# Kernel tuning notes

Measured on AMD Instinct MI355X. Metric: run time of the kernel, lower is better.

The kernel has to match this reference:

```python
import jax, jax.numpy as jnp
import numpy as np

N0, C1, C2 = 100000, 10000, 1000
E0 = 1_600_000
IN = 128
H = 128
OUT = 128


def _pool_edges(ei, ew, cluster, C):
    # PyG pool_edge: remap via cluster, drop self loops, coalesce (sum weights)
    m = cluster[ei]
    mask = m[0] != m[1]
    m = m[:, mask]
    w = ew[mask]
    keys = m[0] * C + m[1]
    uk, inv = np.unique(keys, return_inverse=True)
    w2 = np.bincount(inv, weights=w).astype(np.float32)
    return np.stack([uk // C, uk % C]).astype(np.int64), w2


def _with_self_loops(ei, ew, N):
    # gcn_norm(add_remaining_self_loops, fill_value=1); base edges have no loops
    row = np.concatenate([ei[0], np.arange(N)]).astype(np.int64)
    col = np.concatenate([ei[1], np.arange(N)]).astype(np.int64)
    w = np.concatenate([ew, np.ones(N, np.float32)])
    return row, col, w


def setup_inputs() -> dict:
    rng = np.random.default_rng(0)
    ei = rng.integers(0, N0, size=(2, E0))
    ei = ei[:, ei[0] != ei[1]]
    ew = np.ones(ei.shape[1], np.float32)
    # guaranteed-surjective cluster assignments (stand-in for Louvain output)
    c1 = rng.permutation(np.arange(N0) % C1).astype(np.int64)
    c2 = rng.permutation(np.arange(C1) % C2).astype(np.int64)
    ei1, ew1 = _pool_edges(ei, ew, c1, C1)
    ei2, ew2 = _pool_edges(ei1, ew1, c2, C2)
    r0, co0, w0 = _with_self_loops(ei, ew, N0)
    r1, co1, w1 = _with_self_loops(ei1, ew1, C1)
    r2, co2, w2 = _with_self_loops(ei2, ew2, C2)

    key = jax.random.key(0)
    ks = jax.random.split(key, 16)
    def lin(k, fi, fo):
        return jax.random.normal(k, (fi, fo), jnp.float32) / np.sqrt(fi)
    inp = {
        'x': jax.random.normal(ks[0], (N0, IN), jnp.float32),
        'W_pre': lin(ks[1], IN, H), 'b_pre': jnp.zeros((H,), jnp.float32),
        'W_u0': lin(ks[2], H, H), 'b_u0': jnp.zeros((H,), jnp.float32),
        'W_u1': lin(ks[3], H, H), 'b_u1': jnp.zeros((H,), jnp.float32),
        'W_u2': lin(ks[4], H, H), 'b_u2': jnp.zeros((H,), jnp.float32),
        'W_d0': lin(ks[5], H, OUT), 'b_d0': jnp.zeros((OUT,), jnp.float32),
        'W_d1': lin(ks[6], H, H), 'b_d1': jnp.zeros((H,), jnp.float32),
        'row0': jnp.asarray(r0), 'col0': jnp.asarray(co0), 'ew0': jnp.asarray(w0),
        'row1': jnp.asarray(r1), 'col1': jnp.asarray(co1), 'ew1': jnp.asarray(w1),
        'row2': jnp.asarray(r2), 'col2': jnp.asarray(co2), 'ew2': jnp.asarray(w2),
        'cluster1': jnp.asarray(c1), 'cluster2': jnp.asarray(c2),
    }
    return inp


def _gcn(x, W, b, row, col, ew, N):
    # PyG GCNConv: sym-normalized aggregation at target (col)
    deg = jax.ops.segment_sum(ew, col, num_segments=N)
    dinv = jnp.where(deg > 0, jax.lax.rsqrt(deg), 0.0)
    norm = dinv[row] * ew * dinv[col]
    h = x @ W                                   # [N, F_out]
    out = jax.ops.segment_sum(h[row] * norm[:, None], col, num_segments=N)
    return out + b


def _seg_mean(x, cluster, C):
    s = jax.ops.segment_sum(x, cluster, num_segments=C)
    cnt = jax.ops.segment_sum(jnp.ones((x.shape[0], 1), x.dtype), cluster,
                              num_segments=C)
    return s / jnp.maximum(cnt, 1.0)


def reference(x, W_pre, b_pre, W_u0, b_u0, W_u1, b_u1, W_u2, b_u2,
              W_d0, b_d0, W_d1, b_d1,
              row0, col0, ew0, row1, col1, ew1, row2, col2, ew2,
              cluster1, cluster2):
    # --- up (coarsening) path ---
    h = x @ W_pre + b_pre                                   # preembed
    x0 = jax.nn.relu(_gcn(h, W_u0, b_u0, row0, col0, ew0, N0))
    x1 = _seg_mean(x0, cluster1, C1)                        # avg_pool level 1
    x1 = jax.nn.relu(_gcn(x1, W_u1, b_u1, row1, col1, ew1, C1))
    x2 = _seg_mean(x1, cluster2, C2)                        # avg_pool level 2
    x2 = jax.nn.relu(_gcn(x2, W_u2, b_u2, row2, col2, ew2, C2))
    # --- down (unpooling) path; down convs use all-ones edge weights ---
    y = x1 + x2[cluster2]
    y = jax.nn.relu(_gcn(y, W_d1, b_d1, row1, col1, jnp.ones_like(ew1), C1))
    y = x0 + y[cluster1]
    y = _gcn(y, W_d0, b_d0, row0, col0, jnp.ones_like(ew0), N0)
    return y
```

## Files before the change

### kernel.cpp

```cpp
#include <hip/hip_runtime.h>

#define HH 128
static constexpr int kN0 = 100000;
static constexpr int kC1 = 10000;
static constexpr int kC2 = 1000;

static constexpr int B0 = kN0;
static constexpr int B1 = B0 + kC1;
static constexpr int B2 = B1 + kC2;
static constexpr int B3 = B2 + kC1;
static constexpr int NTOT = B3 + kC2;

static constexpr int NB0 = (kN0 + 127) / 128;
static constexpr int NB1 = (kC1 + 7) / 8;
static constexpr int NB2 = kC2;
static constexpr int NBP1 = (kC1 + 127) / 128;
static constexpr int NBP2 = (kC2 + 15) / 16;
static constexpr int Q0 = NB0;
static constexpr int Q1 = Q0 + NB1;
static constexpr int Q2 = Q1 + NB2;
static constexpr int Q3 = Q2 + NBP1;
static constexpr int NBK = Q3 + NBP2;

__device__ __forceinline__ int bucket_of(int bin) {
  if (bin < B0) return bin >> 7;
  if (bin < B1) return Q0 + ((bin - B0) >> 3);
  if (bin < B2) return Q1 + (bin - B1);
  if (bin < B3) return Q2 + ((bin - B2) >> 7);
  return Q3 + ((bin - B3) >> 4);
}

__device__ __forceinline__ unsigned int f2_to_bf2(float a, float b) {
  unsigned int ua = __float_as_uint(a);
  unsigned int ub = __float_as_uint(b);
  ua = (ua + 0x7fffu + ((ua >> 16) & 1u)) >> 16;
  ub = (ub + 0x7fffu + ((ub >> 16) & 1u)) & 0xffff0000u;
  return ua | ub;
}
__device__ __forceinline__ unsigned short f2bf(float f) {
  unsigned int u = __float_as_uint(f);
  u = (u + 0x7fffu + ((u >> 16) & 1u)) >> 16;
  return (unsigned short)u;
}
__device__ __forceinline__ float bf2f(unsigned short s) {
  return __uint_as_float(((unsigned int)s) << 16);
}

using bf16x8 = __attribute__((ext_vector_type(8))) short;
using f32x4 = __attribute__((ext_vector_type(4))) float;

__global__ __launch_bounds__(256) void p1_kernel(const int* __restrict__ col0,
                                                 const int* __restrict__ col1,
                                                 const int* __restrict__ col2,
                                                 const int* __restrict__ cl1,
                                                 const int* __restrict__ cl2,
                                                 int E0, int E1, int E2,
                                                 int* __restrict__ bucketCnt) {
  __shared__ int h[NBK];
  for (int i = threadIdx.x; i < NBK; i += 256) h[i] = 0;
  __syncthreads();
  int T0 = E0, T1 = T0 + E1, T2 = T1 + E2, T3 = T2 + kN0, T4 = T3 + kC1;
  for (int g = blockIdx.x * 256 + threadIdx.x; g < T4; g += gridDim.x * 256) {
    int bin;
    if (g < T0)      bin = col0[g];
    else if (g < T1) bin = B0 + col1[g - T0];
    else if (g < T2) bin = B1 + col2[g - T1];
    else if (g < T3) bin = B2 + cl1[g - T2];
    else             bin = B3 + cl2[g - T3];
    atomicAdd(&h[bucket_of(bin)], 1);
  }
  __syncthreads();
  for (int i = threadIdx.x; i < NBK; i += 256) {
    int c = h[i];
    if (c) atomicAdd(&bucketCnt[i], c);
  }
}

__global__ __launch_bounds__(1024) void p2_kernel(const int* __restrict__ bucketCnt,
                                                  int* __restrict__ bucketStart,
                                                  int* __restrict__ cursor,
                                                  int* __restrict__ startsg, int T) {
  int t = threadIdx.x;
  int v[4]; int s = 0;
#pragma unroll
  for (int j = 0; j < 4; j++) {
    int i = t * 4 + j;
    v[j] = (i < NBK) ? bucketCnt[i] : 0;
    s += v[j];
  }
  int lane = t & 63, w = t >> 6;
  int incl = s;
  for (int o = 1; o < 64; o <<= 1) { int u = __shfl_up(incl, o); if (lane >= o) incl += u; }
  __shared__ int wt[16];
  if (lane == 63) wt[w] = incl;
  __syncthreads();
  if (t == 0) { int run = 0; for (int i = 0; i < 16; i++) { int c = wt[i]; wt[i] = run; run += c; } }
  __syncthreads();
  int ex = wt[w] + incl - s;
#pragma unroll
  for (int j = 0; j < 4; j++) {
    int i = t * 4 + j;
    if (i < NBK) { bucketStart[i] = ex; cursor[i] = ex; }
    ex += v[j];
  }
  if (t == 0) { bucketStart[NBK] = T; startsg[NTOT] = T; }
}

__global__ __launch_bounds__(256) void p3_kernel(const int* __restrict__ col0,
                                                 const int* __restrict__ col1,
                                                 const int* __restrict__ col2,
                                                 const int* __restrict__ cl1,
                                                 const int* __restrict__ cl2,
                                                 const int* __restrict__ row0,
                                                 const int* __restrict__ row1,
                                                 const int* __restrict__ row2,
                                                 const float* __restrict__ ew1,
                                                 const float* __restrict__ ew2,
                                                 int E0, int E1, int E2,
                                                 int* __restrict__ cursor,
                                                 int4* __restrict__ part) {
  __shared__ int h[NBK];
  __shared__ int gbase[NBK];
  for (int i = threadIdx.x; i < NBK; i += 256) h[i] = 0;
  __syncthreads();
  int T0 = E0, T1 = T0 + E1, T2 = T1 + E2, T3 = T2 + kN0, T4 = T3 + kC1;
  int base = blockIdx.x * 4096;
  int bins[16], srcs[16], rk[16];
  float wv[16];
#pragma unroll
  for (int j = 0; j < 16; j++) {
    int g = base + threadIdx.x + j * 256;
    int bin = -1, src = 0; float w = 0.f;
    if (g < T4) {
      if (g < T0) { bin = col0[g]; src = row0[g]; }
      else if (g < T1) { int e = g - T0; bin = B0 + col1[e]; src = row1[e]; w = ew1[e]; }
      else if (g < T2) { int e = g - T1; bin = B1 + col2[e]; src = row2[e]; w = ew2[e]; }
      else if (g < T3) { int e = g - T2; bin = B2 + cl1[e]; src = e; }
      else             { int e = g - T3; bin = B3 + cl2[e]; src = e; }
    }
    bins[j] = bin; srcs[j] = src; wv[j] = w;
    rk[j] = (bin >= 0) ? atomicAdd(&h[bucket_of(bin)], 1) : 0;
  }
  __syncthreads();
  for (int i = threadIdx.x; i < NBK; i += 256) {
    int c = h[i];
    gbase[i] = c ? atomicAdd(&cursor[i], c) : 0;
  }
  __syncthreads();
#pragma unroll
  for (int j = 0; j < 16; j++) {
    if (bins[j] >= 0) {
      int slot = gbase[bucket_of(bins[j])] + rk[j];
      part[slot] = make_int4(bins[j], srcs[j], __float_as_int(wv[j]), 0);
    }
  }
}

__global__ __launch_bounds__(256) void p4_kernel(const int* __restrict__ bucketStart,
                                                 const int4* __restrict__ part,
                                                 int* __restrict__ startsg,
                                                 int* __restrict__ rowS,
                                                 float* __restrict__ ewSm) {
  int b = blockIdx.x;
  int binLo, width;
  if (b < Q0)      { binLo = b << 7;                 width = 128; if (binLo + width > B0) width = B0 - binLo; }
  else if (b < Q1) { binLo = B0 + ((b - Q0) << 3);   width = 8; }
  else if (b < Q2) { binLo = B1 + (b - Q1);          width = 1; }
  else if (b < Q3) { binLo = B2 + ((b - Q2) << 7);   width = 128; if (binLo + width > B3) width = B3 - binLo; }
  else             { binLo = B3 + ((b - Q3) << 4);   width = 16; if (binLo + width > NTOT) width = NTOT - binLo; }
  int base = bucketStart[b], nend = bucketStart[b + 1];
  int t = threadIdx.x;

  if (width == 1) {
    if (t == 0) startsg[binLo] = base;
    bool isEw = (binLo >= B0 && binLo < B2);
    for (int i = base + t; i < nend; i += 256) {
      int4 it = part[i];
      rowS[i] = it.y;
      if (isEw) ewSm[i] = __int_as_float(it.z);
    }
    return;
  }

  __shared__ int h[128];
  __shared__ int cur[128];
  if (t < 128) h[t] = 0;
  __syncthreads();
  for (int i = base + t; i < nend; i += 256) atomicAdd(&h[part[i].x - binLo], 1);
  __syncthreads();
  if (t == 0) {
    int run = 0;
    for (int j = 0; j < width; j++) {
      cur[j] = run;
      startsg[binLo + j] = base + run;
      run += h[j];
    }
  }
  __syncthreads();
  for (int i = base + t; i < nend; i += 256) {
    int4 it = part[i];
    int k = it.x;
    int r = atomicAdd(&cur[k - binLo], 1);
    int dst = base + r;
    rowS[dst] = it.y;
    if (k >= B0 && k < B2) ewSm[dst] = __int_as_float(it.z);
  }
}

__global__ void dinv_kernel(const int* __restrict__ startsg, const float* __restrict__ ewSm,
                            float* __restrict__ d0, float* __restrict__ d1w,
                            float* __restrict__ d1o, float* __restrict__ d2) {
  int t = blockIdx.x * 256 + threadIdx.x;
  if (t < kN0) {
    int c = startsg[t + 1] - startsg[t];
    d0[t] = c > 0 ? rsqrtf((float)c) : 0.f;
  }
  int wid = t >> 6, lane = t & 63;
  if (wid < kC1) {
    int s = startsg[B0 + wid], e = startsg[B0 + wid + 1];
    float a = 0.f;
    for (int k = s + lane; k < e; k += 64) a += ewSm[k];
    for (int o = 32; o > 0; o >>= 1) a += __shfl_down(a, o);
    if (lane == 0) {
      d1w[wid] = a > 0.f ? rsqrtf(a) : 0.f;
      int c = e - s;
      d1o[wid] = c > 0 ? rsqrtf((float)c) : 0.f;
    }
  } else if (wid < kC1 + kC2) {
    int w2 = wid - kC1;
    int s = startsg[B1 + w2], e = startsg[B1 + w2 + 1];
    float a = 0.f;
    for (int k = s + lane; k < e; k += 64) a += ewSm[k];
    for (int o = 32; o > 0; o >>= 1) a += __shfl_down(a, o);
    if (lane == 0) d2[w2] = a > 0.f ? rsqrtf(a) : 0.f;
  }
}

__global__ void wprep_kernel(const int* __restrict__ rowS, const float* __restrict__ ewSm,
                             const float* __restrict__ d1w, const float* __restrict__ d2,
                             int E0, int E1, int E2,
                             float* __restrict__ wAll) {
  int e = blockIdx.x * 256 + threadIdx.x + E0;
  int tot = E0 + E1 + E2;
  if (e >= tot) return;
  int r = rowS[e];
  if (e < E0 + E1) {
    wAll[e] = d1w[r] * ewSm[e];
  } else {
    wAll[e] = d2[r] * ewSm[e];
  }
}

__global__ __launch_bounds__(256) void matmul_kernel(const float* __restrict__ X,
                                                     const float* __restrict__ Xadd,
                                                     const int* __restrict__ cl,
                                                     const float* __restrict__ W,
                                                     const float* __restrict__ bias,
                                                     const float* __restrict__ rowScale,
                                                     float* __restrict__ Y,
                                                     unsigned int* __restrict__ Ybf, int N) {
  __shared__ float Ws[64 * 128];
  __shared__ float Xs[32 * 128];
  int t = threadIdx.x;
  int rbase = blockIdx.x * 32;
  const float4* X4 = (const float4*)X;
  float4* Xs4 = (float4*)Xs;
#pragma unroll
  for (int i = 0; i < 4; i++) {
    int idx = t + 256 * i;
    int fr = idx >> 5, fc = idx & 31;
    int row = rbase + fr; if (row >= N) row = N - 1;
    float4 v = X4[(size_t)row * 32 + fc];
    if (Xadd) {
      int c = cl[row];
      float4 u = ((const float4*)Xadd)[(size_t)c * 32 + fc];
      v.x += u.x; v.y += u.y; v.z += u.z; v.w += u.w;
    }
    Xs4[idx] = v;
  }
  float acc[4][4];
#pragma unroll
  for (int r = 0; r < 4; r++)
#pragma unroll
    for (int cc = 0; cc < 4; cc++) acc[r][cc] = 0.f;
  int c0 = (t & 31) * 4;
  int rl = (t >> 5) * 4;
  const float4* W4 = (const float4*)W;
  float4* Ws4 = (float4*)Ws;
  for (int half = 0; half < 2; half++) {
    __syncthreads();
#pragma unroll
    for (int i = 0; i < 8; i++) {
      int idx = t + 256 * i;
      Ws4[idx] = W4[half * 2048 + idx];
    }
    __syncthreads();
#pragma unroll 4
    for (int k = 0; k < 64; k++) {
      float4 w4 = *(const float4*)(Ws + k * 128 + c0);
      float xv[4];
#pragma unroll
      for (int r = 0; r < 4; r++) xv[r] = Xs[(rl + r) * 128 + half * 64 + k];
#pragma unroll
      for (int r = 0; r < 4; r++) {
        acc[r][0] = fmaf(xv[r], w4.x, acc[r][0]);
        acc[r][1] = fmaf(xv[r], w4.y, acc[r][1]);
        acc[r][2] = fmaf(xv[r], w4.z, acc[r][2]);
        acc[r][3] = fmaf(xv[r], w4.w, acc[r][3]);
      }
    }
  }
  float4 b4 = make_float4(0.f, 0.f, 0.f, 0.f);
  if (bias) b4 = *(const float4*)(bias + c0);
#pragma unroll
  for (int r = 0; r < 4; r++) {
    int row = rbase + rl + r;
    if (row < N) {
      float sc = rowScale ? rowScale[row] : 1.f;
      float4 o;
      o.x = (acc[r][0] + b4.x) * sc; o.y = (acc[r][1] + b4.y) * sc;
      o.z = (acc[r][2] + b4.z) * sc; o.w = (acc[r][3] + b4.w) * sc;
      if (Ybf) {
        unsigned int pk0 = f2_to_bf2(o.x, o.y);
        unsigned int pk1 = f2_to_bf2(o.z, o.w);
        *(uint2*)(Ybf + (size_t)row * 64 + (c0 >> 1)) = make_uint2(pk0, pk1);
      } else {
        *(float4*)(Y + (size_t)row * 128 + c0) = o;
      }
    }
  }
}

__global__ __launch_bounds__(256, 2) void mfma_gemm_kernel(
    const float* __restrict__ X, const float* __restrict__ Xadd,
    const int* __restrict__ cl, const float* __restrict__ W,
    const float* __restrict__ bias, const float* __restrict__ rowScale,
    unsigned int* __restrict__ Ybf, int N) {
  __shared__ unsigned int Bt[128 * 64];
  int t = threadIdx.x;
  {
    int n = t & 127, kh = t >> 7;
#pragma unroll
    for (int k = kh * 64; k < kh * 64 + 64; k += 2) {
      float a = W[(size_t)k * 128 + n];
      float b = W[(size_t)(k + 1) * 128 + n];
      unsigned int pk = (unsigned int)f2bf(a) | ((unsigned int)f2bf(b) << 16);
      unsigned int byteoff = ((unsigned int)(n * 256 + k * 2)) ^ (((unsigned int)n & 7u) << 4);
      *(unsigned int*)((char*)Bt + byteoff) = pk;
    }
  }
  __syncthreads();
  int wv = t >> 6, lane = t & 63;
  int g = lane >> 4, mrow = lane & 15;
  int rbase = blockIdx.x * 128 + wv * 32;
  bf16x8 ahi[2][4], alo[2][4];
#pragma unroll
  for (int mt = 0; mt < 2; mt++) {
    int row = rbase + mt * 16 + mrow;
    int rc = row < N ? row : N - 1;
    const float4* Xr = (const float4*)(X + (size_t)rc * 128);
    const float4* Ar = Xadd ? (const float4*)(Xadd + (size_t)cl[rc] * 128) : nullptr;
#pragma unroll
    for (int ks = 0; ks < 4; ks++) {
      int c4 = ks * 8 + g * 2;
      float4 v0 = Xr[c4], v1 = Xr[c4 + 1];
      if (Ar) {
        float4 u0 = Ar[c4], u1 = Ar[c4 + 1];
        v0.x += u0.x; v0.y += u0.y; v0.z += u0.z; v0.w += u0.w;
        v1.x += u1.x; v1.y += u1.y; v1.z += u1.z; v1.w += u1.w;
      }
      float vv[8] = {v0.x, v0.y, v0.z, v0.w, v1.x, v1.y, v1.z, v1.w};
      bf16x8 h, l;
#pragma unroll
      for (int j = 0; j < 8; j++) {
        unsigned short hb = f2bf(vv[j]);
        h[j] = (short)hb;
        l[j] = (short)f2bf(vv[j] - bf2f(hb));
      }
      ahi[mt][ks] = h; alo[mt][ks] = l;
    }
  }
  f32x4 acc[2][8];
#pragma unroll
  for (int mt = 0; mt < 2; mt++)
#pragma unroll
    for (int nt = 0; nt < 8; nt++) acc[mt][nt] = (f32x4){0.f, 0.f, 0.f, 0.f};
#pragma unroll
  for (int ks = 0; ks < 4; ks++) {
#pragma unroll
    for (int nt = 0; nt < 8; nt++) {
      int n = nt * 16 + mrow;
      unsigned int byteoff =
          ((unsigned int)(n * 256 + ks * 64 + g * 16)) ^ (((unsigned int)n & 7u) << 4);
      bf16x8 b = *(const bf16x8*)((const char*)Bt + byteoff);
      acc[0][nt] = __builtin_amdgcn_mfma_f32_16x16x32_bf16(ahi[0][ks], b, acc[0][nt], 0, 0, 0);
      acc[1][nt] = __builtin_amdgcn_mfma_f32_16x16x32_bf16(ahi[1][ks], b, acc[1][nt], 0, 0, 0);
      acc[0][nt] = __builtin_amdgcn_mfma_f32_16x16x32_bf16(alo[0][ks], b, acc[0][nt], 0, 0, 0);
      acc[1][nt] = __builtin_amdgcn_mfma_f32_16x16x32_bf16(alo[1][ks], b, acc[1][nt], 0, 0, 0);
    }
  }
#pragma unroll
  for (int mt = 0; mt < 2; mt++) {
#pragma unroll
    for (int r = 0; r < 4; r++) {
      int row = rbase + mt * 16 + g * 4 + r;
      if (row < N) {
        float sc = rowScale ? rowScale[row] : 1.f;
#pragma unroll
        for (int nt = 0; nt < 4; nt++) {
          int c = nt * 16 + mrow;
          float lo = (acc[mt][nt][r] + (bias ? bias[c] : 0.f)) * sc;
          float hi = (acc[mt][nt + 4][r] + (bias ? bias[c + 64] : 0.f)) * sc;
          Ybf[(size_t)row * 64 + c] = (unsigned int)f2bf(lo) | ((unsigned int)f2bf(hi) << 16);
        }
      }
    }
  }
}

__global__ __launch_bounds__(256) void agg_kernel(const unsigned int* __restrict__ Hf,
                                                  float* __restrict__ out,
                                                  const int* __restrict__ starts,
                                                  const int* __restrict__ rowS,
                                                  const float* __restrict__ dinv,
                                                  const float* __restrict__ bias,
                                                  int C, int relu) {
  int wid = (blockIdx.x * blockDim.x + threadIdx.x) >> 6;
  int lane = threadIdx.x & 63;
  if (wid >= C) return;
  int s = starts[wid], e = starts[wid + 1];
  float dc = dinv[wid];
  float ax[4] = {0.f, 0.f, 0.f, 0.f}, ay[4] = {0.f, 0.f, 0.f, 0.f};
  for (int base = s; base < e; base += 64) {
    int n = e - base; if (n > 64) n = 64;
    int r = rowS[base + (lane < n ? lane : 0)];
    int j = 0;
    for (; j + 7 < n; j += 8) {
#pragma unroll
      for (int u = 0; u < 8; u++) {
        int rr = __shfl(r, j + u);
        unsigned int pv = Hf[(size_t)rr * 64 + lane];
        ax[u & 3] += __uint_as_float(pv << 16);
        ay[u & 3] += __uint_as_float(pv & 0xffff0000u);
      }
    }
    for (; j < n; j++) {
      int rr = __shfl(r, j);
      unsigned int pv = Hf[(size_t)rr * 64 + lane];
      ax[0] += __uint_as_float(pv << 16);
      ay[0] += __uint_as_float(pv & 0xffff0000u);
    }
  }
  float ox = (ax[0] + ax[1] + ax[2] + ax[3]) * dc + bias[lane];
  float oy = (ay[0] + ay[1] + ay[2] + ay[3]) * dc + bias[64 + lane];
  if (relu) { ox = fmaxf(ox, 0.f); oy = fmaxf(oy, 0.f); }
  out[(size_t)wid * 128 + lane] = ox;
  out[(size_t)wid * 128 + 64 + lane] = oy;
}

__global__ __launch_bounds__(256) void aggb_kernel(const unsigned int* __restrict__ Hf,
                                                   float* __restrict__ out,
                                                   const int* __restrict__ starts,
                                                   const int* __restrict__ rowS,
                                                   const float* __restrict__ wS,
                                                   const float* __restrict__ dinv,
                                                   const float* __restrict__ bias,
                                                   int C, int relu) {
  int node = blockIdx.x;
  if (node >= C) return;
  int wv = threadIdx.x >> 6, lane = threadIdx.x & 63;
  int s = starts[node], e = starts[node + 1];
  float ax[4] = {0.f, 0.f, 0.f, 0.f}, ay[4] = {0.f, 0.f, 0.f, 0.f};
  for (int base = s + wv * 64; base < e; base += 256) {
    int n = e - base; if (n > 64) n = 64;
    int moff = base + (lane < n ? lane : 0);
    int r = rowS[moff];
    float w = wS[moff];
    int j = 0;
    for (; j + 7 < n; j += 8) {
#pragma unroll
      for (int u = 0; u < 8; u++) {
        int rr = __shfl(r, j + u);
        float ww = __shfl(w, j + u);
        unsigned int pv = Hf[(size_t)rr * 64 + lane];
        ax[u & 3] = fmaf(ww, __uint_as_float(pv << 16), ax[u & 3]);
        ay[u & 3] = fmaf(ww, __uint_as_float(pv & 0xffff0000u), ay[u & 3]);
      }
    }
    for (; j < n; j++) {
      int rr = __shfl(r, j);
      float ww = __shfl(w, j);
      unsigned int pv = Hf[(size_t)rr * 64 + lane];
      ax[0] = fmaf(ww, __uint_as_float(pv << 16), ax[0]);
      ay[0] = fmaf(ww, __uint_as_float(pv & 0xffff0000u), ay[0]);
    }
  }
  __shared__ float shx[256], shy[256];
  shx[threadIdx.x] = ax[0] + ax[1] + ax[2] + ax[3];
  shy[threadIdx.x] = ay[0] + ay[1] + ay[2] + ay[3];
  __syncthreads();
  if (threadIdx.x < 64) {
    float sx = shx[lane] + shx[lane + 64] + shx[lane + 128] + shx[lane + 192];
    float sy = shy[lane] + shy[lane + 64] + shy[lane + 128] + shy[lane + 192];
    float dc = dinv[node];
    float ox = sx * dc + bias[lane * 2];
    float oy = sy * dc + bias[lane * 2 + 1];
    if (relu) { ox = fmaxf(ox, 0.f); oy = fmaxf(oy, 0.f); }
    *(float2*)(out + (size_t)node * 128 + lane * 2) = make_float2(ox, oy);
  }
}

__global__ __launch_bounds__(256) void aggb1_kernel(const unsigned int* __restrict__ Hf,
                                                    float* __restrict__ out,
                                                    const int* __restrict__ starts,
                                                    const int* __restrict__ rowS,
                                                    const float* __restrict__ dinv,
                                                    const float* __restrict__ bias,
                                                    int C, int relu) {
  int node = blockIdx.x;
  if (node >= C) return;
  int wv = threadIdx.x >> 6, lane = threadIdx.x & 63;
  int s = starts[node], e = starts[node + 1];
  float ax[4] = {0.f, 0.f, 0.f, 0.f}, ay[4] = {0.f, 0.f, 0.f, 0.f};
  for (int base = s + wv * 64; base < e; base += 256) {
    int n = e - base; if (n > 64) n = 64;
    int r = rowS[base + (lane < n ? lane : 0)];
    int j = 0;
    for (; j + 7 < n; j += 8) {
#pragma unroll
      for (int u = 0; u < 8; u++) {
        int rr = __shfl(r, j + u);
        unsigned int pv = Hf[(size_t)rr * 64 + lane];
        ax[u & 3] += __uint_as_float(pv << 16);
        ay[u & 3] += __uint_as_float(pv & 0xffff0000u);
      }
    }
    for (; j < n; j++) {
      int rr = __shfl(r, j);
      unsigned int pv = Hf[(size_t)rr * 64 + lane];
      ax[0] += __uint_as_float(pv << 16);
      ay[0] += __uint_as_float(pv & 0xffff0000u);
    }
  }
  __shared__ float shx[256], shy[256];
  shx[threadIdx.x] = ax[0] + ax[1] + ax[2] + ax[3];
  shy[threadIdx.x] = ay[0] + ay[1] + ay[2] + ay[3];
  __syncthreads();
  if (threadIdx.x < 64) {
    float sx = shx[lane] + shx[lane + 64] + shx[lane + 128] + shx[lane + 192];
    float sy = shy[lane] + shy[lane + 64] + shy[lane + 128] + shy[lane + 192];
    float dc = dinv[node];
    float ox = sx * dc + bias[lane * 2];
    float oy = sy * dc + bias[lane * 2 + 1];
    if (relu) { ox = fmaxf(ox, 0.f); oy = fmaxf(oy, 0.f); }
    *(float2*)(out + (size_t)node * 128 + lane * 2) = make_float2(ox, oy);
  }
}

__global__ __launch_bounds__(256) void pool_kernel(const float* __restrict__ src,
                                                   float* __restrict__ out,
                                                   const int* __restrict__ starts,
                                                   const int* __restrict__ rowS, int C) {
  int wid = (blockIdx.x * blockDim.x + threadIdx.x) >> 6;
  int lane = threadIdx.x & 63;
  if (wid >= C) return;
  int s = starts[wid], e = starts[wid + 1];
  float ax0 = 0.f, ay0 = 0.f, ax1 = 0.f, ay1 = 0.f;
  int m = s;
  for (; m + 3 < e; m += 4) {
    int i0 = rowS[m], i1 = rowS[m + 1], i2 = rowS[m + 2], i3 = rowS[m + 3];
    float2 v0 = *(const float2*)(src + (size_t)i0 * 128 + lane * 2);
    float2 v1 = *(const float2*)(src + (size_t)i1 * 128 + lane * 2);
    float2 v2 = *(const float2*)(src + (size_t)i2 * 128 + lane * 2);
    float2 v3 = *(const float2*)(src + (size_t)i3 * 128 + lane * 2);
    ax0 += v0.x; ay0 += v0.y;
    ax1 += v1.x; ay1 += v1.y;
    ax0 += v2.x; ay0 += v2.y;
    ax1 += v3.x; ay1 += v3.y;
  }
  for (; m < e; m++) {
    int id = rowS[m];
    const float2 v = *(const float2*)(src + (size_t)id * 128 + lane * 2);
    ax0 += v.x; ay0 += v.y;
  }
  float inv = (e > s) ? 1.f / (float)(e - s) : 0.f;
  *(float2*)(out + (size_t)wid * 128 + lane * 2) =
      make_float2((ax0 + ax1) * inv, (ay0 + ay1) * inv);
}


extern "C" void kernel_launch(void* const* d_in, const int* in_sizes, int n_in,
                              void* d_out, int out_size, void* d_ws, size_t ws_size,
                              hipStream_t stream) {
  const float* x     = (const float*)d_in[0];
  const float* W_pre = (const float*)d_in[1];
  const float* b_pre = (const float*)d_in[2];
  const float* W_u0  = (const float*)d_in[3];
  const float* b_u0  = (const float*)d_in[4];
  const float* W_u1  = (const float*)d_in[5];
  const float* b_u1  = (const float*)d_in[6];
  const float* W_u2  = (const float*)d_in[7];
  const float* b_u2  = (const float*)d_in[8];
  const float* W_d0  = (const float*)d_in[9];
  const float* b_d0  = (const float*)d_in[10];
  const float* W_d1  = (const float*)d_in[11];
  const float* b_d1  = (const float*)d_in[12];
  const int* row0 = (const int*)d_in[13];
  const int* col0 = (const int*)d_in[14];
  const int* row1 = (const int*)d_in[16];
  const int* col1 = (const int*)d_in[17];
  const float* ew1 = (const float*)d_in[18];
  const int* row2 = (const int*)d_in[19];
  const int* col2 = (const int*)d_in[20];
  const float* ew2 = (const float*)d_in[21];
  const int* cluster1 = (const int*)d_in[22];
  const int* cluster2 = (const int*)d_in[23];
  int E0 = in_sizes[13], E1 = in_sizes[16], E2 = in_sizes[19];
  float* out = (float*)d_out;
  int Ttot = E0 + E1 + E2 + kN0 + kC1;
  int Etot = E0 + E1 + E2;

  char* basep = (char*)d_ws;
  size_t off = 0;
  auto alloc = [&](size_t bytes) -> char* {
    char* p = basep + off;
    off = (off + bytes + 255) & ~(size_t)255;
    return p;
  };
  int* bucketCnt = (int*)alloc((size_t)NBK * 4);
  size_t zero_bytes = off;
  int* bucketStart = (int*)alloc((size_t)(NBK + 1) * 4);
  int* cursor      = (int*)alloc((size_t)NBK * 4);
  int* startsg     = (int*)alloc((size_t)(NTOT + 1) * 4);
  int* rowS  = (int*)alloc((size_t)Ttot * 4);
  float* ewS = (float*)alloc((size_t)(E1 + E2) * 4);
  float* ewSm = ewS - E0;
  float* dinv0  = (float*)alloc((size_t)kN0 * 4);
  float* dinv1w = (float*)alloc((size_t)kC1 * 4);
  float* dinv1o = (float*)alloc((size_t)kC1 * 4);
  float* dinv2  = (float*)alloc((size_t)kC2 * 4);
  size_t watermark = off;
  int4* part = (int4*)alloc((size_t)Ttot * 16);
  off = watermark;
  float* wAll = (float*)alloc((size_t)Etot * 4);
  float* Wf   = (float*)alloc((size_t)128 * 128 * 4);
  float* bfv  = (float*)alloc((size_t)128 * 4);
  float* A    = (float*)alloc((size_t)kN0 * HH * 4);
  float* s1a  = (float*)alloc((size_t)kC1 * HH * 4);
  float* s1b  = (float*)alloc((size_t)kC1 * HH * 4);
  float* s2a  = (float*)alloc((size_t)kC2 * HH * 4);
  unsigned int* s1bb = (unsigned int*)alloc((size_t)kC1 * 64 * 4);
  unsigned int* s2bb = (unsigned int*)alloc((size_t)kC2 * 64 * 4);
  unsigned int* s1cb = (unsigned int*)alloc((size_t)kC1 * 64 * 4);
  unsigned int* tb   = (unsigned int*)alloc((size_t)kN0 * 64 * 4);
  unsigned int* t0   = (unsigned int*)d_out;

  hipMemsetAsync(d_ws, 0, zero_bytes, stream);

  auto cdiv = [](int a, int b) { return (a + b - 1) / b; };

  p1_kernel<<<256, 256, 0, stream>>>(col0, col1, col2, cluster1, cluster2, E0, E1, E2, bucketCnt);
  p2_kernel<<<1, 1024, 0, stream>>>(bucketCnt, bucketStart, cursor, startsg, Ttot);
  p3_kernel<<<cdiv(Ttot, 4096), 256, 0, stream>>>(col0, col1, col2, cluster1, cluster2,
                                                  row0, row1, row2, ew1, ew2, E0, E1, E2,
                                                  cursor, part);
  p4_kernel<<<NBK, 256, 0, stream>>>(bucketStart, part, startsg, rowS, ewSm);
  dinv_kernel<<<cdiv((kC1 + kC2) * 64, 256), 256, 0, stream>>>(startsg, ewSm, dinv0, dinv1w,
                                                               dinv1o, dinv2);
  wprep_kernel<<<cdiv(E1 + E2, 256), 256, 0, stream>>>(rowS, ewSm, dinv1w, dinv2,
                                                       E0, E1, E2, wAll);

  matmul_kernel<<<cdiv(128, 32), 256, 0, stream>>>(W_pre, nullptr, nullptr, W_u0, nullptr,
                                                   nullptr, Wf, nullptr, 128);
  matmul_kernel<<<1, 256, 0, stream>>>(b_pre, nullptr, nullptr, W_u0, nullptr,
                                       nullptr, bfv, nullptr, 1);
  mfma_gemm_kernel<<<cdiv(kN0, 128), 256, 0, stream>>>(x, nullptr, nullptr, Wf, bfv, dinv0,
                                                       t0, kN0);
  agg_kernel<<<cdiv(kN0, 4), 256, 0, stream>>>(t0, A, startsg, rowS, dinv0, b_u0, kN0, 1);
  pool_kernel<<<cdiv(kC1, 4), 256, 0, stream>>>(A, s1a, startsg + B2, rowS, kC1);
  matmul_kernel<<<cdiv(kC1, 32), 256, 0, stream>>>(s1a, nullptr, nullptr, W_u1, nullptr,
                                                   nullptr, nullptr, s1bb, kC1);
  aggb_kernel<<<kC1, 256, 0, stream>>>(s1bb, s1a, startsg + B0, rowS, wAll, dinv1w, b_u1, kC1, 1);
  pool_kernel<<<cdiv(kC2, 4), 256, 0, stream>>>(s1a, s2a, startsg + B3, rowS, kC2);
  matmul_kernel<<<cdiv(kC2, 32), 256, 0, stream>>>(s2a, nullptr, nullptr, W_u2, nullptr,
                                                   nullptr, nullptr, s2bb, kC2);
  aggb_kernel<<<kC2, 256, 0, stream>>>(s2bb, s2a, startsg + B1, rowS, wAll, dinv2, b_u2, kC2, 1);
  matmul_kernel<<<cdiv(kC1, 32), 256, 0, stream>>>(s1a, s2a, cluster2, W_d1, nullptr,
                                                   dinv1o, nullptr, s1cb, kC1);
  aggb1_kernel<<<kC1, 256, 0, stream>>>(s1cb, s1b, startsg + B0, rowS, dinv1o, b_d1, kC1, 1);
  mfma_gemm_kernel<<<cdiv(kN0, 128), 256, 0, stream>>>(A, s1b, cluster1, W_d0, nullptr, dinv0,
                                                       tb, kN0);
  agg_kernel<<<cdiv(kN0, 4), 256, 0, stream>>>(tb, out, startsg, rowS, dinv0, b_d0, kN0, 0);
}
```

Measured before the change: 660.5 us.

## Split partition buffer, widen agg gathers to two edges per wave, deepen unrolls

The bucket partition buffer moves from int4 records to an int2 bin/src array plus a separate weight array. This cuts the bytes written and read in the sort passes, since weights are only read for the weighted levels. The main N0 aggregation now has each half-wave gather a different edge with 8-byte loads and combines the halves with a cross-lane shuffle, giving more memory parallelism per wave. Other aggregation and pool loops unroll deeper (16 and 8 edges), which raises loads in flight at the cost of more registers.

```diff
diff --git a/kernel.cpp b/kernel.cpp
--- a/kernel.cpp
+++ b/kernel.cpp
@@ -118,7 +118,8 @@
                                                  const float* __restrict__ ew2,
                                                  int E0, int E1, int E2,
                                                  int* __restrict__ cursor,
-                                                 int4* __restrict__ part) {
+                                                 int2* __restrict__ partBS,
+                                                 float* __restrict__ partW) {
   __shared__ int h[NBK];
   __shared__ int gbase[NBK];
   for (int i = threadIdx.x; i < NBK; i += 256) h[i] = 0;
@@ -151,13 +152,15 @@
   for (int j = 0; j < 16; j++) {
     if (bins[j] >= 0) {
       int slot = gbase[bucket_of(bins[j])] + rk[j];
-      part[slot] = make_int4(bins[j], srcs[j], __float_as_int(wv[j]), 0);
+      partBS[slot] = make_int2(bins[j], srcs[j]);
+      partW[slot] = wv[j];
     }
   }
 }
 
 __global__ __launch_bounds__(256) void p4_kernel(const int* __restrict__ bucketStart,
-                                                 const int4* __restrict__ part,
+                                                 const int2* __restrict__ partBS,
+                                                 const float* __restrict__ partW,
                                                  int* __restrict__ startsg,
                                                  int* __restrict__ rowS,
                                                  float* __restrict__ ewSm) {
@@ -170,14 +173,14 @@
   else             { binLo = B3 + ((b - Q3) << 4);   width = 16; if (binLo + width > NTOT) width = NTOT - binLo; }
   int base = bucketStart[b], nend = bucketStart[b + 1];
   int t = threadIdx.x;
+  bool isEw = (binLo >= B0 && binLo < B2);
 
   if (width == 1) {
     if (t == 0) startsg[binLo] = base;
-    bool isEw = (binLo >= B0 && binLo < B2);
     for (int i = base + t; i < nend; i += 256) {
-      int4 it = part[i];
+      int2 it = partBS[i];
       rowS[i] = it.y;
-      if (isEw) ewSm[i] = __int_as_float(it.z);
+      if (isEw) ewSm[i] = partW[i];
     }
     return;
   }
@@ -186,7 +189,7 @@
   __shared__ int cur[128];
   if (t < 128) h[t] = 0;
   __syncthreads();
-  for (int i = base + t; i < nend; i += 256) atomicAdd(&h[part[i].x - binLo], 1);
+  for (int i = base + t; i < nend; i += 256) atomicAdd(&h[partBS[i].x - binLo], 1);
   __syncthreads();
   if (t == 0) {
     int run = 0;
@@ -198,12 +201,11 @@
   }
   __syncthreads();
   for (int i = base + t; i < nend; i += 256) {
-    int4 it = part[i];
-    int k = it.x;
-    int r = atomicAdd(&cur[k - binLo], 1);
+    int2 it = partBS[i];
+    int r = atomicAdd(&cur[it.x - binLo], 1);
     int dst = base + r;
     rowS[dst] = it.y;
-    if (k >= B0 && k < B2) ewSm[dst] = __int_as_float(it.z);
+    if (isEw) ewSm[dst] = partW[i];
   }
 }
 
@@ -428,34 +430,36 @@
   int wid = (blockIdx.x * blockDim.x + threadIdx.x) >> 6;
   int lane = threadIdx.x & 63;
   if (wid >= C) return;
+  int h = lane >> 5, hl = lane & 31;
+  const uint2* Hf2 = (const uint2*)Hf;
   int s = starts[wid], e = starts[wid + 1];
   float dc = dinv[wid];
-  float ax[4] = {0.f, 0.f, 0.f, 0.f}, ay[4] = {0.f, 0.f, 0.f, 0.f};
+  float a0 = 0.f, a1 = 0.f, b0 = 0.f, b1 = 0.f;
   for (int base = s; base < e; base += 64) {
     int n = e - base; if (n > 64) n = 64;
     int r = rowS[base + (lane < n ? lane : 0)];
-    int j = 0;
-    for (; j + 7 < n; j += 8) {
+    for (int j = 0; j < n; j += 16) {
 #pragma unroll
       for (int u = 0; u < 8; u++) {
-        int rr = __shfl(r, j + u);
-        unsigned int pv = Hf[(size_t)rr * 64 + lane];
-        ax[u & 3] += __uint_as_float(pv << 16);
-        ay[u & 3] += __uint_as_float(pv & 0xffff0000u);
-      }
-    }
-    for (; j < n; j++) {
-      int rr = __shfl(r, j);
-      unsigned int pv = Hf[(size_t)rr * 64 + lane];
-      ax[0] += __uint_as_float(pv << 16);
-      ay[0] += __uint_as_float(pv & 0xffff0000u);
-    }
-  }
-  float ox = (ax[0] + ax[1] + ax[2] + ax[3]) * dc + bias[lane];
-  float oy = (ay[0] + ay[1] + ay[2] + ay[3]) * dc + bias[64 + lane];
-  if (relu) { ox = fmaxf(ox, 0.f); oy = fmaxf(oy, 0.f); }
-  out[(size_t)wid * 128 + lane] = ox;
-  out[(size_t)wid * 128 + 64 + lane] = oy;
+        int eidx = j + u * 2 + h;
+        bool v = eidx < n;
+        int rr = __shfl(r, v ? eidx : 0);
+        uint2 pv = Hf2[(size_t)rr * 32 + hl];
+        if (!v) { pv.x = 0u; pv.y = 0u; }
+        a0 += __uint_as_float(pv.x << 16);
+        b0 += __uint_as_float(pv.x & 0xffff0000u);
+        a1 += __uint_as_float(pv.y << 16);
+        b1 += __uint_as_float(pv.y & 0xffff0000u);
+      }
+    }
+  }
+  a0 += __shfl_xor(a0, 32); a1 += __shfl_xor(a1, 32);
+  b0 += __shfl_xor(b0, 32); b1 += __shfl_xor(b1, 32);
+  int c0 = h * 64 + hl * 2;
+  float o0 = (h ? b0 : a0) * dc + bias[c0];
+  float o1 = (h ? b1 : a1) * dc + bias[c0 + 1];
+  if (relu) { o0 = fmaxf(o0, 0.f); o1 = fmaxf(o1, 0.f); }
+  *(float2*)(out + (size_t)wid * 128 + c0) = make_float2(o0, o1);
 }
 
 __global__ __launch_bounds__(256) void aggb_kernel(const unsigned int* __restrict__ Hf,
@@ -477,9 +481,9 @@
     int r = rowS[moff];
     float w = wS[moff];
     int j = 0;
-    for (; j + 7 < n; j += 8) {
-#pragma unroll
-      for (int u = 0; u < 8; u++) {
+    for (; j + 15 < n; j += 16) {
+#pragma unroll
+      for (int u = 0; u < 16; u++) {
         int rr = __shfl(r, j + u);
         float ww = __shfl(w, j + u);
         unsigned int pv = Hf[(size_t)rr * 64 + lane];
@@ -526,9 +530,9 @@
     int n = e - base; if (n > 64) n = 64;
     int r = rowS[base + (lane < n ? lane : 0)];
     int j = 0;
-    for (; j + 7 < n; j += 8) {
-#pragma unroll
-      for (int u = 0; u < 8; u++) {
+    for (; j + 15 < n; j += 16) {
+#pragma unroll
+      for (int u = 0; u < 16; u++) {
         int rr = __shfl(r, j + u);
         unsigned int pv = Hf[(size_t)rr * 64 + lane];
         ax[u & 3] += __uint_as_float(pv << 16);
@@ -567,16 +571,15 @@
   int s = starts[wid], e = starts[wid + 1];
   float ax0 = 0.f, ay0 = 0.f, ax1 = 0.f, ay1 = 0.f;
   int m = s;
-  for (; m + 3 < e; m += 4) {
-    int i0 = rowS[m], i1 = rowS[m + 1], i2 = rowS[m + 2], i3 = rowS[m + 3];
-    float2 v0 = *(const float2*)(src + (size_t)i0 * 128 + lane * 2);
-    float2 v1 = *(const float2*)(src + (size_t)i1 * 128 + lane * 2);
-    float2 v2 = *(const float2*)(src + (size_t)i2 * 128 + lane * 2);
-    float2 v3 = *(const float2*)(src + (size_t)i3 * 128 + lane * 2);
-    ax0 += v0.x; ay0 += v0.y;
-    ax1 += v1.x; ay1 += v1.y;
-    ax0 += v2.x; ay0 += v2.y;
-    ax1 += v3.x; ay1 += v3.y;
+  for (; m + 7 < e; m += 8) {
+    int idx[8];
+#pragma unroll
+    for (int u = 0; u < 8; u++) idx[u] = rowS[m + u];
+#pragma unroll
+    for (int u = 0; u < 8; u++) {
+      float2 v = *(const float2*)(src + (size_t)idx[u] * 128 + lane * 2);
+      if (u & 1) { ax1 += v.x; ay1 += v.y; } else { ax0 += v.x; ay0 += v.y; }
+    }
   }
   for (; m < e; m++) {
     int id = rowS[m];
@@ -640,7 +643,8 @@
   float* dinv1o = (float*)alloc((size_t)kC1 * 4);
   float* dinv2  = (float*)alloc((size_t)kC2 * 4);
   size_t watermark = off;
-  int4* part = (int4*)alloc((size_t)Ttot * 16);
+  int2* partBS = (int2*)alloc((size_t)Ttot * 8);
+  float* partW = (float*)alloc((size_t)Ttot * 4);
   off = watermark;
   float* wAll = (float*)alloc((size_t)Etot * 4);
   float* Wf   = (float*)alloc((size_t)128 * 128 * 4);
@@ -663,8 +667,8 @@
   p2_kernel<<<1, 1024, 0, stream>>>(bucketCnt, bucketStart, cursor, startsg, Ttot);
   p3_kernel<<<cdiv(Ttot, 4096), 256, 0, stream>>>(col0, col1, col2, cluster1, cluster2,
                                                   row0, row1, row2, ew1, ew2, E0, E1, E2,
-                                                  cursor, part);
-  p4_kernel<<<NBK, 256, 0, stream>>>(bucketStart, part, startsg, rowS, ewSm);
+                                                  cursor, partBS, partW);
+  p4_kernel<<<NBK, 256, 0, stream>>>(bucketStart, partBS, partW, startsg, rowS, ewSm);
   dinv_kernel<<<cdiv((kC1 + kC2) * 64, 256), 256, 0, stream>>>(startsg, ewSm, dinv0, dinv1w,
                                                                dinv1o, dinv2);
   wprep_kernel<<<cdiv(E1 + E2, 256), 256, 0, stream>>>(rowS, ewSm, dinv1w, dinv2,
```

Measured after the change: 687.1 us. 4.0% more time.
